# Optimization experiments

Hardware: AMD Instinct MI355X
Metric: run time of the kernel (lower is better)

The kernel has to match this reference:

```python
import jax, jax.numpy as jnp
import numpy as np

NEG = -1e9

def setup_inputs() -> dict:
    key = jax.random.key(0)
    kx, kq, kk, kv, kbq, kbk, kbv = jax.random.split(key, 7)
    B, S, E, D = 4, 2048, 1024, 64
    x = jax.random.normal(kx, (B, S, E), dtype=jnp.float32)
    # causal mask, broadcast over batch (mask == 0 positions get -1e9)
    mask = jnp.broadcast_to(jnp.tril(jnp.ones((S, S), dtype=jnp.int32)), (B, S, S))
    scale = 1.0 / np.sqrt(E)
    Wq = jax.random.normal(kq, (E, D), dtype=jnp.float32) * scale
    Wk = jax.random.normal(kk, (E, D), dtype=jnp.float32) * scale
    Wv = jax.random.normal(kv, (E, D), dtype=jnp.float32) * scale
    bq = jnp.zeros((D,), dtype=jnp.float32)
    bk = jnp.zeros((D,), dtype=jnp.float32)
    bv = jnp.zeros((D,), dtype=jnp.float32)
    return {"x": x, "mask": mask, "Wq": Wq, "bq": bq, "Wk": Wk, "bk": bk, "Wv": Wv, "bv": bv}

def reference(x, mask, Wq, bq, Wk, bk, Wv, bv):
    # Faithful to original: forward passes (K(x), Q(x), V(x)) into sdpa,
    # so the K-projection plays the 'query' role and Q-projection the 'key' role.
    q = jnp.einsum('bse,ed->bsd', x, Wk) + bk  # K(x) used as queries
    k = jnp.einsum('bse,ed->bsd', x, Wq) + bq  # Q(x) used as keys
    v = jnp.einsum('bse,ed->bsd', x, Wv) + bv
    d = q.shape[-1]
    scores = jnp.einsum('bsd,btd->bst', q, k) / jnp.sqrt(jnp.asarray(d, q.dtype))
    scores = jnp.where(mask == 0, jnp.asarray(NEG, scores.dtype), scores)
    weights = jax.nn.softmax(scores, axis=-1)
    return jnp.einsum('bst,btd->bsd', weights, v)
```

## Files before the change

### kernel.cpp

```cpp
#include <hip/hip_runtime.h>

typedef short bf16x8 __attribute__((ext_vector_type(8)));
typedef float f32x4  __attribute__((ext_vector_type(4)));
typedef int   i32x4  __attribute__((ext_vector_type(4)));

#define NEG_BIG (-1e9f)

__device__ __forceinline__ float bf2f(unsigned short h){
  union { unsigned u; float f; } v; v.u = ((unsigned)h) << 16; return v.f;
}
__device__ __forceinline__ unsigned short f2bf(float f){
  union { float f; unsigned u; } v; v.f = f;
  unsigned u = v.u;
  return (unsigned short)((u + 0x7FFFu + ((u >> 16) & 1u)) >> 16);
}

__global__ __launch_bounds__(256) void prep_kernel(
    const float* __restrict__ Wq, const float* __restrict__ bq,
    const float* __restrict__ Wk, const float* __restrict__ bk,
    const float* __restrict__ Wv, const float* __restrict__ bv,
    unsigned short* __restrict__ Wimg, float* __restrict__ bias,
    unsigned int* __restrict__ tick)
{
  int idx = blockIdx.x * 256 + threadIdx.x;
  if (idx < 192 * 1024) {
    int kb2 = idx / 24576, rem = idx % 24576;
    int r = rem >> 7, kk = rem & 127;
    int k = kb2 * 128 + kk;
    float v;
    if (r < 64)       v = Wk[k * 64 + r];
    else if (r < 128) v = Wq[k * 64 + (r - 64)];
    else              v = Wv[k * 64 + (r - 128)];
    Wimg[kb2 * 24576 + r * 128 + kk] = f2bf(v);
  }
  if (idx < 192) {
    float b;
    if (idx < 64)       b = bk[idx];
    else if (idx < 128) b = bq[idx - 64];
    else                b = bv[idx - 128];
    bias[idx] = b;
  }
  if (idx < 128) tick[idx] = 0u;
}

__global__ __launch_bounds__(256, 2) void proj_kernel(
    const float* __restrict__ x,
    const unsigned short* __restrict__ Wimg,
    const float* __restrict__ bias,
    unsigned short* __restrict__ Qh,
    unsigned short* __restrict__ Kh, unsigned short* __restrict__ Vth)
{
  __shared__ __align__(16) unsigned short Axb[32 * 128];
  __shared__ __align__(16) unsigned short Wc[96 * 128];

  const int tid  = threadIdx.x;
  const int lane = tid & 63;
  const int w    = tid >> 6;
  const int rh   = w & 1;
  const int cg   = w >> 1;
  const int quad = lane >> 4;
  const int li   = lane & 15;
  const int rowbase = (blockIdx.x >> 1) * 32;
  const int ch      = blockIdx.x & 1;

  const int xr0 = tid >> 4,          xc0 = tid & 15;
  const int xr1 = (tid + 256) >> 4,  xc1 = tid & 15;
  const float* agp0 = x + (size_t)(rowbase + xr0) * 1024 + xc0 * 8;
  const float* agp1 = x + (size_t)(rowbase + xr1) * 1024 + xc1 * 8;
  const int aslot0 = xr0 * 128 + (xc0 ^ (xr0 & 15)) * 8;
  const int aslot1 = xr1 * 128 + (xc1 ^ (xr1 & 15)) * 8;

  int wslot[6];
  const unsigned short* wgp[6];
  #pragma unroll
  for (int j = 0; j < 6; j++) {
    int cid = tid + j * 256;
    int wr = cid >> 4, c = cid & 15;
    wslot[j] = wr * 128 + (c ^ (wr & 15)) * 8;
    wgp[j] = Wimg + (size_t)(ch * 96 + wr) * 128 + c * 8;
  }

  f32x4 acc[3];
  #pragma unroll
  for (int c = 0; c < 3; c++) acc[c] = (f32x4){0.f, 0.f, 0.f, 0.f};

  const int alr = rh * 16 + li;

  f32x4 rA[4];
  rA[0] = *(const f32x4*)(agp0);
  rA[1] = *(const f32x4*)(agp0 + 4);
  rA[2] = *(const f32x4*)(agp1);
  rA[3] = *(const f32x4*)(agp1 + 4);
  i32x4 rW[6];
  #pragma unroll
  for (int j = 0; j < 6; j++) rW[j] = *(const i32x4*)(wgp[j]);

  for (int ks = 0; ks < 8; ks++) {
    bf16x8 xa, xb;
    #pragma unroll
    for (int j = 0; j < 4; j++) {
      xa[j]     = f2bf(rA[0][j]);
      xa[4 + j] = f2bf(rA[1][j]);
      xb[j]     = f2bf(rA[2][j]);
      xb[4 + j] = f2bf(rA[3][j]);
    }
    __syncthreads();
    *(bf16x8*)&Axb[aslot0] = xa;
    *(bf16x8*)&Axb[aslot1] = xb;
    #pragma unroll
    for (int j = 0; j < 6; j++) *(i32x4*)&Wc[wslot[j]] = rW[j];
    if (ks < 7) {
      rA[0] = *(const f32x4*)(agp0 + (ks + 1) * 128);
      rA[1] = *(const f32x4*)(agp0 + (ks + 1) * 128 + 4);
      rA[2] = *(const f32x4*)(agp1 + (ks + 1) * 128);
      rA[3] = *(const f32x4*)(agp1 + (ks + 1) * 128 + 4);
      #pragma unroll
      for (int j = 0; j < 6; j++)
        rW[j] = *(const i32x4*)(wgp[j] + (size_t)(ks + 1) * 24576);
    }
    __syncthreads();

    #pragma unroll
    for (int sub = 0; sub < 4; sub++) {
      bf16x8 af = *(const bf16x8*)&Axb[alr * 128 + ((sub * 4 + quad) ^ (alr & 15)) * 8];
      #pragma unroll
      for (int ct = 0; ct < 3; ct++) {
        const int lw = cg * 48 + ct * 16 + li;
        bf16x8 bf = *(const bf16x8*)&Wc[lw * 128 + ((sub * 4 + quad) ^ (lw & 15)) * 8];
        acc[ct] = __builtin_amdgcn_mfma_f32_16x16x32_bf16(af, bf, acc[ct], 0, 0, 0);
      }
    }
  }

  #pragma unroll
  for (int ct = 0; ct < 3; ct++)
    #pragma unroll
    for (int r = 0; r < 4; r++) {
      int row = rowbase + rh * 16 + quad * 4 + r;
      int col = ch * 96 + cg * 48 + ct * 16 + li;
      unsigned short h = f2bf(acc[ct][r] + bias[col]);
      if (col < 64)        Qh[(size_t)row * 64 + col] = h;
      else if (col < 128)  Kh[(size_t)row * 64 + (col - 64)] = h;
      else {
        int d = col - 128; int bb = row >> 11; int s = row & 2047;
        Vth[(size_t)bb * 131072 + (size_t)d * 2048 + s] = h;
      }
    }
}

__global__ __launch_bounds__(256, 3) void attn_kernel(
    const unsigned short* __restrict__ Qh,
    const unsigned short* __restrict__ Kh,
    const unsigned short* __restrict__ Vth,
    float* __restrict__ pacc, float* __restrict__ pl,
    unsigned int* __restrict__ tick, float* __restrict__ out)
{
  __shared__ __align__(16) unsigned short Ps[4][16 * 72];
  __shared__ unsigned int lastflag;

  const int tid  = threadIdx.x;
  const int lane = tid & 63;
  const int w    = tid >> 6;
  const int quad = lane >> 4;
  const int li   = lane & 15;

  const int b = blockIdx.x / 144;
  int r = blockIdx.x % 144;
  int qg = 31, part = 0;
  #pragma unroll 1
  for (int g = 31; g >= 0; g--) {
    int Pg = (g + 4) >> 2;
    if (r < Pg) { qg = g; part = r; break; }
    r -= Pg;
  }
  const int nkt = qg + 1;
  const int P   = (qg + 4) >> 2;
  const int base = nkt / P, rem = nkt % P;
  const int kt0 = part * base + (part < rem ? part : rem);
  const int kt1 = kt0 + base + (part < rem ? 1 : 0);
  const int qbase = qg * 64 + w * 16;

  size_t qoff = ((size_t)(b * 2048 + qbase) + li) * 64 + quad * 8;
  bf16x8 qh0 = *(const bf16x8*)(Qh + qoff);
  bf16x8 qh1 = *(const bf16x8*)(Qh + qoff + 32);

  f32x4 acc[4];
  #pragma unroll
  for (int c = 0; c < 4; c++) acc[c] = (f32x4){0.f, 0.f, 0.f, 0.f};
  f32x4 lacc = (f32x4){0.f, 0.f, 0.f, 0.f};

  bf16x8 ones;
  #pragma unroll
  for (int j = 0; j < 8; j++) ones[j] = (short)0x3F80;

  const unsigned short* Kb = Kh  + (size_t)b * (2048 * 64);
  const unsigned short* Vb = Vth + (size_t)b * 131072;
  int koff[4], voff[4];
  #pragma unroll
  for (int ct = 0; ct < 4; ct++) {
    koff[ct] = (ct * 16 + li) * 64   + quad * 8;
    voff[ct] = (ct * 16 + li) * 2048 + quad * 8;
  }

  for (int kt = kt0; kt < kt1; kt++) {
    const unsigned short* Kt = Kb + kt * 4096;
    const unsigned short* Vt = Vb + kt * 64;

    bf16x8 vf0[4], vf1[4];
    #pragma unroll
    for (int ct = 0; ct < 4; ct++) {
      vf0[ct] = *(const bf16x8*)(Vt + voff[ct]);
      vf1[ct] = *(const bf16x8*)(Vt + voff[ct] + 32);
    }

    f32x4 s[4];
    #pragma unroll
    for (int c = 0; c < 4; c++) s[c] = (f32x4){0.f, 0.f, 0.f, 0.f};

    __builtin_amdgcn_s_setprio(1);
    #pragma unroll
    for (int ct = 0; ct < 4; ct++) {
      bf16x8 kf0 = *(const bf16x8*)(Kt + koff[ct]);
      bf16x8 kf1 = *(const bf16x8*)(Kt + koff[ct] + 32);
      s[ct] = __builtin_amdgcn_mfma_f32_16x16x32_bf16(qh0, kf0, s[ct], 0, 0, 0);
      s[ct] = __builtin_amdgcn_mfma_f32_16x16x32_bf16(qh1, kf1, s[ct], 0, 0, 0);
    }
    __builtin_amdgcn_s_setprio(0);

    const bool diag = (kt == qg);
    const int kb = kt * 64;
    #pragma unroll
    for (int ct = 0; ct < 4; ct++)
      #pragma unroll
      for (int rr = 0; rr < 4; rr++) {
        float t = fmaf(s[ct][rr], 0.18033688011112042f, -23.083120654223414f);
        if (diag && (kb + ct * 16 + li > qbase + quad * 4 + rr)) t = -1e30f;
        Ps[w][(quad * 4 + rr) * 72 + ct * 16 + li] = f2bf(exp2f(t));
      }

    bf16x8 ap0 = *(const bf16x8*)&Ps[w][li * 72 + quad * 8];
    bf16x8 ap1 = *(const bf16x8*)&Ps[w][li * 72 + 32 + quad * 8];

    __builtin_amdgcn_s_setprio(1);
    lacc = __builtin_amdgcn_mfma_f32_16x16x32_bf16(ap0, ones, lacc, 0, 0, 0);
    lacc = __builtin_amdgcn_mfma_f32_16x16x32_bf16(ap1, ones, lacc, 0, 0, 0);
    #pragma unroll
    for (int ct = 0; ct < 4; ct++) {
      acc[ct] = __builtin_amdgcn_mfma_f32_16x16x32_bf16(ap0, vf0[ct], acc[ct], 0, 0, 0);
      acc[ct] = __builtin_amdgcn_mfma_f32_16x16x32_bf16(ap1, vf1[ct], acc[ct], 0, 0, 0);
    }
    __builtin_amdgcn_s_setprio(0);
  }

  if (P == 1) {
    float inv[4];
    #pragma unroll
    for (int rr = 0; rr < 4; rr++) inv[rr] = 1.0f / lacc[rr];
    #pragma unroll
    for (int ct = 0; ct < 4; ct++)
      #pragma unroll
      for (int rr = 0; rr < 4; rr++)
        out[(size_t)(b * 2048 + qg * 64 + w * 16 + quad * 4 + rr) * 64 + ct * 16 + li]
          = acc[ct][rr] * inv[rr];
    return;
  }

  const int slot = (b * 32 + qg) * 8 + part;
  float* pa = pacc + (size_t)slot * 4096;
  #pragma unroll
  for (int ct = 0; ct < 4; ct++)
    #pragma unroll
    for (int rr = 0; rr < 4; rr++)
      pa[(w * 16 + quad * 4 + rr) * 64 + ct * 16 + li] = acc[ct][rr];
  if (li == 0) {
    #pragma unroll
    for (int rr = 0; rr < 4; rr++)
      pl[slot * 64 + w * 16 + quad * 4 + rr] = lacc[rr];
  }

  __syncthreads();
  if (tid == 0) {
    __threadfence();
    lastflag = (atomicAdd(tick + (b * 32 + qg), 1u) == (unsigned)(P - 1)) ? 1u : 0u;
  }
  __syncthreads();
  if (!lastflag) return;
  __builtin_amdgcn_fence(__ATOMIC_ACQUIRE, "agent");

  const int mr = tid >> 2;
  const int c0 = (tid & 3) * 16;
  const int slot0 = (b * 32 + qg) * 8;
  f32x4 a0 = (f32x4){0.f,0.f,0.f,0.f}, a1 = a0, a2 = a0, a3 = a0;
  float L = 0.f;
  for (int p = 0; p < P; p++) {
    const float* q = pacc + (size_t)(slot0 + p) * 4096 + mr * 64 + c0;
    a0 += *(const f32x4*)(q);
    a1 += *(const f32x4*)(q + 4);
    a2 += *(const f32x4*)(q + 8);
    a3 += *(const f32x4*)(q + 12);
    L += pl[(slot0 + p) * 64 + mr];
  }
  float inv = 1.f / L;
  float* o = out + ((size_t)(b * 2048 + qg * 64 + mr)) * 64 + c0;
  *(f32x4*)(o)      = a0 * inv;
  *(f32x4*)(o + 4)  = a1 * inv;
  *(f32x4*)(o + 8)  = a2 * inv;
  *(f32x4*)(o + 12) = a3 * inv;
}

extern "C" void kernel_launch(void* const* d_in, const int* in_sizes, int n_in,
                              void* d_out, int out_size, void* d_ws, size_t ws_size,
                              hipStream_t stream)
{
  (void)in_sizes; (void)n_in; (void)out_size; (void)ws_size;
  const float* x  = (const float*)d_in[0];
  const float* Wq = (const float*)d_in[2];
  const float* bq = (const float*)d_in[3];
  const float* Wk = (const float*)d_in[4];
  const float* bk = (const float*)d_in[5];
  const float* Wv = (const float*)d_in[6];
  const float* bv = (const float*)d_in[7];
  float* out = (float*)d_out;

  char* ws = (char*)d_ws;
  const size_t MB = 1u << 20;
  unsigned short* Qh   = (unsigned short*)(ws);
  unsigned short* Kh   = (unsigned short*)(ws + 2 * MB);
  unsigned short* Vth  = (unsigned short*)(ws + 4 * MB);
  unsigned short* Wimg = (unsigned short*)(ws + 6 * MB);
  float*          bias = (float*)(ws + 6 * MB + 786432);
  float*          pacc = (float*)(ws + 8 * MB);
  float*          pl   = (float*)(ws + 25 * MB);
  unsigned int*   tick = (unsigned int*)(ws + 26 * MB);

  prep_kernel<<<dim3(768), dim3(256), 0, stream>>>(Wq, bq, Wk, bk, Wv, bv, Wimg, bias, tick);
  proj_kernel<<<dim3(512), dim3(256), 0, stream>>>(x, Wimg, bias, Qh, Kh, Vth);
  attn_kernel<<<dim3(576), dim3(256), 0, stream>>>(Qh, Kh, Vth, pacc, pl, tick, out);
}
```

Before: 183.6 us.

## Stage K/V tiles in swizzled shared memory with register prefetch

Each block now loads the 64x64 K and V tiles cooperatively into XOR-swizzled LDS buffers once per iteration. Before, each of the four waves read K and V fragments straight from global memory, duplicating the traffic. The next tile is prefetched into registers while the current one is computed, which hides global latency. In exchange there are two __syncthreads per iteration and 16KB more LDS per block, which may reduce occupancy relative to the launch bound of 3 blocks.

```diff
diff --git a/kernel.cpp b/kernel.cpp
--- a/kernel.cpp
+++ b/kernel.cpp
@@ -155,6 +155,8 @@
     float* __restrict__ pacc, float* __restrict__ pl,
     unsigned int* __restrict__ tick, float* __restrict__ out)
 {
+  __shared__ __align__(16) unsigned short Kst[64 * 64];
+  __shared__ __align__(16) unsigned short Vst[64 * 64];
   __shared__ __align__(16) unsigned short Ps[4][16 * 72];
   __shared__ unsigned int lastflag;
 
@@ -193,35 +195,40 @@
   #pragma unroll
   for (int j = 0; j < 8; j++) ones[j] = (short)0x3F80;
 
-  const unsigned short* Kb = Kh  + (size_t)b * (2048 * 64);
-  const unsigned short* Vb = Vth + (size_t)b * 131072;
-  int koff[4], voff[4];
-  #pragma unroll
-  for (int ct = 0; ct < 4; ct++) {
-    koff[ct] = (ct * 16 + li) * 64   + quad * 8;
-    voff[ct] = (ct * 16 + li) * 2048 + quad * 8;
-  }
+  const int srow = tid >> 2, sc = tid & 3;
+  const unsigned short* kgp = Kh + (size_t)(b * 2048 + srow) * 64 + sc * 8;
+  const unsigned short* vgp = Vth + (size_t)b * 131072 + (size_t)srow * 2048 + sc * 8;
+  const int ks0 = srow * 64 + ((sc)     ^ (srow & 7)) * 8;
+  const int ks1 = srow * 64 + ((sc + 4) ^ (srow & 7)) * 8;
+
+  i32x4 rk0 = *(const i32x4*)(kgp + (size_t)kt0 * 4096);
+  i32x4 rk1 = *(const i32x4*)(kgp + (size_t)kt0 * 4096 + 32);
+  i32x4 rv0 = *(const i32x4*)(vgp + kt0 * 64);
+  i32x4 rv1 = *(const i32x4*)(vgp + kt0 * 64 + 32);
 
   for (int kt = kt0; kt < kt1; kt++) {
-    const unsigned short* Kt = Kb + kt * 4096;
-    const unsigned short* Vt = Vb + kt * 64;
-
-    bf16x8 vf0[4], vf1[4];
+    __syncthreads();
+    *(i32x4*)&Kst[ks0] = rk0;
+    *(i32x4*)&Kst[ks1] = rk1;
+    *(i32x4*)&Vst[ks0] = rv0;
+    *(i32x4*)&Vst[ks1] = rv1;
+    if (kt + 1 < kt1) {
+      rk0 = *(const i32x4*)(kgp + (size_t)(kt + 1) * 4096);
+      rk1 = *(const i32x4*)(kgp + (size_t)(kt + 1) * 4096 + 32);
+      rv0 = *(const i32x4*)(vgp + (kt + 1) * 64);
+      rv1 = *(const i32x4*)(vgp + (kt + 1) * 64 + 32);
+    }
+    __syncthreads();
+
+    f32x4 s[4];
+    #pragma unroll
+    for (int c = 0; c < 4; c++) s[c] = (f32x4){0.f, 0.f, 0.f, 0.f};
+    __builtin_amdgcn_s_setprio(1);
     #pragma unroll
     for (int ct = 0; ct < 4; ct++) {
-      vf0[ct] = *(const bf16x8*)(Vt + voff[ct]);
-      vf1[ct] = *(const bf16x8*)(Vt + voff[ct] + 32);
-    }
-
-    f32x4 s[4];
-    #pragma unroll
-    for (int c = 0; c < 4; c++) s[c] = (f32x4){0.f, 0.f, 0.f, 0.f};
-
-    __builtin_amdgcn_s_setprio(1);
-    #pragma unroll
-    for (int ct = 0; ct < 4; ct++) {
-      bf16x8 kf0 = *(const bf16x8*)(Kt + koff[ct]);
-      bf16x8 kf1 = *(const bf16x8*)(Kt + koff[ct] + 32);
+      const int n = ct * 16 + li;
+      bf16x8 kf0 = *(const bf16x8*)&Kst[n * 64 + ((quad)     ^ (n & 7)) * 8];
+      bf16x8 kf1 = *(const bf16x8*)&Kst[n * 64 + ((quad + 4) ^ (n & 7)) * 8];
       s[ct] = __builtin_amdgcn_mfma_f32_16x16x32_bf16(qh0, kf0, s[ct], 0, 0, 0);
       s[ct] = __builtin_amdgcn_mfma_f32_16x16x32_bf16(qh1, kf1, s[ct], 0, 0, 0);
     }
@@ -246,8 +253,11 @@
     lacc = __builtin_amdgcn_mfma_f32_16x16x32_bf16(ap1, ones, lacc, 0, 0, 0);
     #pragma unroll
     for (int ct = 0; ct < 4; ct++) {
-      acc[ct] = __builtin_amdgcn_mfma_f32_16x16x32_bf16(ap0, vf0[ct], acc[ct], 0, 0, 0);
-      acc[ct] = __builtin_amdgcn_mfma_f32_16x16x32_bf16(ap1, vf1[ct], acc[ct], 0, 0, 0);
+      const int n = ct * 16 + li;
+      bf16x8 vf0 = *(const bf16x8*)&Vst[n * 64 + ((quad)     ^ (n & 7)) * 8];
+      bf16x8 vf1 = *(const bf16x8*)&Vst[n * 64 + ((quad + 4) ^ (n & 7)) * 8];
+      acc[ct] = __builtin_amdgcn_mfma_f32_16x16x32_bf16(ap0, vf0, acc[ct], 0, 0, 0);
+      acc[ct] = __builtin_amdgcn_mfma_f32_16x16x32_bf16(ap1, vf1, acc[ct], 0, 0, 0);
     }
     __builtin_amdgcn_s_setprio(0);
   }
```

Result: faster. 173.1 us (-5.7%).
